# Kernel tuning notes

Measured on AMD Instinct MI355X. Metric: run time of the kernel, lower is better.

The kernel has to match this reference:

```python
import jax, jax.numpy as jnp
import numpy as np

D = 768; H = 12; NL = 8; V = 128
LATENT = 1024; TA = 1000; L = 90; S = 1120; B = 8
PAD_IDX = 0


def sinu_pos(n, dim):
    # ScaledSinusoidalEmbedding basis (scale applied by caller)
    half = dim // 2
    inv_freq = 10000.0 ** (-(jnp.arange(half, dtype=jnp.float32) / half))
    ang = jnp.arange(n, dtype=jnp.float32)[:, None] * inv_freq[None, :]
    return jnp.concatenate([jnp.sin(ang), jnp.cos(ang)], axis=-1)  # [n, dim]


def ln(x, g):
    m = x.mean(-1, keepdims=True)
    v = ((x - m) ** 2).mean(-1, keepdims=True)
    return (x - m) * jax.lax.rsqrt(v + 1e-5) * g


def decoder(x, ln1_g, ln2_g, lnf_g, qkv_w, attn_o_w, fc_w, mlp_o_w):
    Bq, Sq, _ = x.shape
    dh = D // H
    causal = jnp.tril(jnp.ones((Sq, Sq), bool))
    for l in range(NL):
        h = ln(x, ln1_g[l])
        q, k, v = jnp.split(h @ qkv_w[l].T, 3, axis=-1)
        q = q.reshape(Bq, Sq, H, dh).transpose(0, 2, 1, 3)
        k = k.reshape(Bq, Sq, H, dh).transpose(0, 2, 1, 3)
        v = v.reshape(Bq, Sq, H, dh).transpose(0, 2, 1, 3)
        att = jnp.einsum('bhqd,bhkd->bhqk', q, k) / jnp.sqrt(jnp.asarray(dh, x.dtype))
        att = jax.nn.softmax(jnp.where(causal, att, -1e9), axis=-1)
        o = jnp.einsum('bhqk,bhkd->bhqd', att, v).transpose(0, 2, 1, 3).reshape(Bq, Sq, D)
        x = x + o @ attn_o_w[l].T
        h = ln(x, ln2_g[l])
        x = x + jax.nn.gelu(h @ fc_w[l].T, approximate=False) @ mlp_o_w[l].T
    return ln(x, lnf_g)


def setup_inputs() -> dict:
    key = jax.random.key(0)
    ks = iter(jax.random.split(key, 24))
    p = lambda shape: 0.02 * jax.random.normal(next(ks), shape, jnp.float32)
    inp = {}
    inp['audio'] = jax.random.normal(next(ks), (B, TA, LATENT), jnp.float32)
    inp['audio_lengths'] = jax.random.randint(next(ks), (B,), TA // 2, TA + 1)
    ll = jax.random.randint(next(ks), (B,), L // 2, L + 1)
    ll = ll.at[0].set(L)  # labels are padded to max label length in-batch
    inp['label_lengths'] = ll
    lab = jax.random.randint(next(ks), (B, L), 2, V)
    inp['labels'] = jnp.where(jnp.arange(L)[None, :] < ll[:, None], lab, PAD_IDX)
    inp['text_emb_w'] = p((V, D))
    inp['text_head_w'] = p((V, D))
    inp['audio_proj_w'] = p((D, LATENT))
    inp['audio_proj_b'] = jnp.zeros((D,), jnp.float32)
    inp['start_emb'] = p((D,))
    inp['audio_pos_scale'] = jnp.asarray(D ** -0.5, jnp.float32)
    inp['text_pos_scale'] = jnp.asarray(D ** -0.5, jnp.float32)
    inp['ln1_g'] = jnp.ones((NL, D), jnp.float32)
    inp['ln2_g'] = jnp.ones((NL, D), jnp.float32)
    inp['lnf_g'] = jnp.ones((D,), jnp.float32)
    inp['qkv_w'] = p((NL, 3 * D, D))
    inp['attn_o_w'] = p((NL, D, D))
    inp['fc_w'] = p((NL, 4 * D, D))
    inp['mlp_o_w'] = p((NL, D, 4 * D))
    return inp


def reference(audio, labels, audio_lengths, label_lengths, text_emb_w, text_head_w,
              audio_proj_w, audio_proj_b, start_emb, audio_pos_scale, text_pos_scale,
              ln1_g, ln2_g, lnf_g, qkv_w, attn_o_w, fc_w, mlp_o_w):
    # audio projection + scaled sinusoidal positions
    audio_h = audio @ audio_proj_w.T + audio_proj_b                  # [B,TA,D]
    audio_h = audio_h + sinu_pos(TA, D) * audio_pos_scale
    text_h = text_emb_w[labels] + sinu_pos(L, D) * text_pos_scale    # [B,L,D]

    # vectorized ragged packing: [audio[:al] | start_emb | text[:ll-1] | zero-pad] -> [B,S,D]
    pos = jnp.arange(S)[None, :]                                     # [1,S]
    al = audio_lengths[:, None]
    ll = label_lengths[:, None]
    aud = jnp.pad(audio_h, ((0, 0), (0, S - TA), (0, 0)))
    tj = jnp.clip(pos - al - 1, 0, L - 1)                            # text index per slot
    txt = jnp.take_along_axis(text_h, tj[:, :, None], axis=1)
    emb = jnp.where((pos < al)[..., None], aud,
          jnp.where((pos == al)[..., None], start_emb,
          jnp.where((pos < al + ll)[..., None], txt, 0.0)))

    x = decoder(emb, ln1_g, ln2_g, lnf_g, qkv_w, attn_o_w, fc_w, mlp_o_w)

    # gather text latents x[b, al:al+ll] padded to L (== labels.shape[1])
    j = jnp.arange(L)[None, :]
    gi = jnp.clip(al + j, 0, S - 1)
    lat = jnp.take_along_axis(x, gi[:, :, None], axis=1)             # [B,L,D]
    lat = jnp.where((j < ll)[..., None], lat, 0.0)
    logits = lat @ text_head_w.T                                     # [B,L,V]

    # cross entropy, ignore_index = PAD_IDX, mean over non-pad tokens
    logp = jax.nn.log_softmax(logits, axis=-1)
    nll = -jnp.take_along_axis(logp, labels[..., None], axis=-1)[..., 0]
    m = (labels != PAD_IDX).astype(jnp.float32)
    return jnp.sum(nll * m) / jnp.sum(m)
```

## Files before the change

### kernel.cpp

```cpp
#include <hip/hip_runtime.h>

#define D_   768
#define H_   12
#define NL_  8
#define V_   128
#define LAT_ 1024
#define TA_  1000
#define L_   90
#define S_   1120
#define B_   8
#define DH_  64
#define MROWS (B_*S_)

typedef __bf16 bf16x8_t __attribute__((ext_vector_type(8)));
typedef float  f32x4_t  __attribute__((ext_vector_type(4)));

__global__ void sniff_kernel(const void* __restrict__ ones_src,
                             int* __restrict__ flag, float* __restrict__ accum) {
  if (threadIdx.x == 0) {
    unsigned w = *(const unsigned*)ones_src;
    flag[0] = (w == 0x3F803F80u) ? 1 : 0;
    accum[0] = 0.0f;
    accum[1] = 0.0f;
  }
}

__global__ __launch_bounds__(256) void cvt8_kernel(const void* __restrict__ src,
    long off, __bf16* __restrict__ dst, long n8, const int* __restrict__ flag) {
  long i = (long)blockIdx.x * 256 + threadIdx.x;
  const long stride = (long)gridDim.x * 256;
  if (*flag) {
    const bf16x8_t* s = (const bf16x8_t*)((const __bf16*)src + off);
    bf16x8_t* d = (bf16x8_t*)dst;
    for (; i < n8; i += stride) d[i] = s[i];
  } else {
    const float* s = (const float*)src + off;
    for (; i < n8; i += stride) {
      float4 a = *(const float4*)(s + i*8);
      float4 b = *(const float4*)(s + i*8 + 4);
      bf16x8_t v;
      v[0]=(__bf16)a.x; v[1]=(__bf16)a.y; v[2]=(__bf16)a.z; v[3]=(__bf16)a.w;
      v[4]=(__bf16)b.x; v[5]=(__bf16)b.y; v[6]=(__bf16)b.z; v[7]=(__bf16)b.w;
      *(bf16x8_t*)(dst + i*8) = v;
    }
  }
}

__global__ void cvt1_kernel(const void* __restrict__ src, long off,
    __bf16* __restrict__ dst, int n, const int* __restrict__ flag) {
  int i = threadIdx.x;
  if (i < n) {
    if (*flag) dst[i] = ((const __bf16*)src + off)[i];
    else       dst[i] = (__bf16)((const float*)src + off)[i];
  }
}

__device__ __forceinline__ void gload_lds16(const __bf16* g, __bf16* l) {
  __builtin_amdgcn_global_load_lds(
      (const __attribute__((address_space(1))) void*)g,
      (__attribute__((address_space(3))) void*)l, 16, 0, 0);
}

template<int EPI>
__global__ __launch_bounds__(256) void gemm_kernel(
    const __bf16* __restrict__ A, const __bf16* __restrict__ W,
    void* __restrict__ Cout, const __bf16* __restrict__ bias,
    int M, int N, int K)
{
  __shared__ __align__(16) __bf16 As[128*32];
  __shared__ __align__(16) __bf16 Ws[128*32];
  const int tid  = threadIdx.x;
  const int wave = tid >> 6, lane = tid & 63;
  const int wm = wave >> 1, wn = wave & 1;
  const int lrow = lane & 15, lquad = lane >> 4;
  const int bm = blockIdx.y * 128, bn = blockIdx.x * 128;

  const int c0    = wave*2;
  const int srow0 = c0*16 + (lane >> 2);
  const int kc8   = (lane & 3) * 8;
  const int gaA0  = min(bm + srow0,      M-1);
  const int gaA1  = min(bm + srow0 + 16, M-1);
  const size_t a0 = (size_t)gaA0*K + kc8;
  const size_t a1 = (size_t)gaA1*K + kc8;
  const size_t w0 = (size_t)(bn + srow0)*K + kc8;
  const size_t w1 = (size_t)(bn + srow0 + 16)*K + kc8;
  __bf16* ldsA0 = &As[ c0   *512 + lane*8];
  __bf16* ldsA1 = &As[(c0+1)*512 + lane*8];
  __bf16* ldsW0 = &Ws[ c0   *512 + lane*8];
  __bf16* ldsW1 = &Ws[(c0+1)*512 + lane*8];

  f32x4_t acc[4][4] = {};

  for (int kk = 0; kk < K; kk += 32) {
    gload_lds16(&A[a0 + kk], ldsA0);
    gload_lds16(&A[a1 + kk], ldsA1);
    gload_lds16(&W[w0 + kk], ldsW0);
    gload_lds16(&W[w1 + kk], ldsW1);
    __syncthreads();

    bf16x8_t af[4], bfr[4];
    #pragma unroll
    for (int i = 0; i < 4; ++i)
      af[i] = *reinterpret_cast<const bf16x8_t*>(&As[(wm*64 + i*16 + lrow)*32 + lquad*8]);
    #pragma unroll
    for (int j = 0; j < 4; ++j)
      bfr[j] = *reinterpret_cast<const bf16x8_t*>(&Ws[(wn*64 + j*16 + lrow)*32 + lquad*8]);
    #pragma unroll
    for (int i = 0; i < 4; ++i)
      #pragma unroll
      for (int j = 0; j < 4; ++j)
        acc[i][j] = __builtin_amdgcn_mfma_f32_16x16x32_bf16(af[i], bfr[j], acc[i][j], 0, 0, 0);
    __syncthreads();
  }

  const int orow0 = bm + wm*64 + lquad*4;
  const int ocol0 = bn + wn*64 + lrow;
  #pragma unroll
  for (int i = 0; i < 4; ++i) {
    #pragma unroll
    for (int j = 0; j < 4; ++j) {
      #pragma unroll
      for (int r = 0; r < 4; ++r) {
        int row = orow0 + i*16 + r;
        int col = ocol0 + j*16;
        if (row < M) {
          float v = acc[i][j][r];
          if (EPI == 0) {
            ((__bf16*)Cout)[(size_t)row*N + col] = (__bf16)v;
          } else if (EPI == 1) {
            ((float*)Cout)[(size_t)row*N + col] = v + (float)bias[col];
          } else if (EPI == 2) {
            ((float*)Cout)[(size_t)row*N + col] += v;
          } else {
            float gv = 0.5f * v * (1.0f + erff(v * 0.70710678118654752f));
            ((__bf16*)Cout)[(size_t)row*N + col] = (__bf16)gv;
          }
        }
      }
    }
  }
}

template<bool F32OUT>
__global__ __launch_bounds__(256) void ln_kernel(const float* __restrict__ x,
    const __bf16* __restrict__ g, void* __restrict__ outp)
{
  const int row = blockIdx.x;
  const int tid = threadIdx.x;
  const float* xr = x + (size_t)row * D_;
  float v0 = xr[tid], v1 = xr[tid+256], v2 = xr[tid+512];
  float s  = v0+v1+v2;
  float sq = v0*v0 + v1*v1 + v2*v2;
  #pragma unroll
  for (int off = 32; off > 0; off >>= 1) {
    s  += __shfl_down(s,  off);
    sq += __shfl_down(sq, off);
  }
  __shared__ float ps[4], pq[4];
  __shared__ float smean, srstd;
  const int wave = tid >> 6, lane = tid & 63;
  if (lane == 0) { ps[wave] = s; pq[wave] = sq; }
  __syncthreads();
  if (tid == 0) {
    float S4 = ps[0]+ps[1]+ps[2]+ps[3];
    float Q4 = pq[0]+pq[1]+pq[2]+pq[3];
    float mean = S4 * (1.0f/D_);
    float var  = Q4 * (1.0f/D_) - mean*mean;
    smean = mean;
    srstd = rsqrtf(var + 1e-5f);
  }
  __syncthreads();
  const float mean = smean, rstd = srstd;
  if (F32OUT) {
    float* o = (float*)outp + (size_t)row*D_;
    o[tid]     = (v0-mean)*rstd*(float)g[tid];
    o[tid+256] = (v1-mean)*rstd*(float)g[tid+256];
    o[tid+512] = (v2-mean)*rstd*(float)g[tid+512];
  } else {
    __bf16* o = (__bf16*)outp + (size_t)row*D_;
    o[tid]     = (__bf16)((v0-mean)*rstd*(float)g[tid]);
    o[tid+256] = (__bf16)((v1-mean)*rstd*(float)g[tid+256]);
    o[tid+512] = (__bf16)((v2-mean)*rstd*(float)g[tid+512]);
  }
}

__device__ __forceinline__ float sinu_pe(int pindex, int d) {
  int d2 = (d < 384) ? d : d - 384;
  float invf = __expf(-((float)d2 / 384.0f) * 9.210340371976184f);
  float ang  = (float)pindex * invf;
  return (d < 384) ? sinf(ang) : cosf(ang);
}

__global__ __launch_bounds__(256) void embed_kernel(const float* __restrict__ audio_h,
    const int* __restrict__ labels, const int* __restrict__ alen, const int* __restrict__ llen,
    const __bf16* __restrict__ temb, const __bf16* __restrict__ semb,
    const __bf16* __restrict__ aps, const __bf16* __restrict__ tps,
    float* __restrict__ x)
{
  const int bp = blockIdx.x;
  const int b = bp / S_, pos = bp % S_;
  const int a = alen[b], t = llen[b];
  float* xr = x + (size_t)bp * D_;
  if (pos < a) {
    const float apsf = (float)aps[0];
    const float* ar = audio_h + ((size_t)b*TA_ + pos)*D_;
    for (int d = threadIdx.x; d < D_; d += 256)
      xr[d] = ar[d] + sinu_pe(pos, d) * apsf;
  } else if (pos == a) {
    for (int d = threadIdx.x; d < D_; d += 256) xr[d] = (float)semb[d];
  } else if (pos < a + t) {
    const float tpsf = (float)tps[0];
    int tj = pos - a - 1;
    tj = tj < 0 ? 0 : (tj > L_-1 ? L_-1 : tj);
    int tok = labels[b*L_ + tj];
    const __bf16* tr = temb + (size_t)tok * D_;
    for (int d = threadIdx.x; d < D_; d += 256)
      xr[d] = (float)tr[d] + sinu_pe(tj, d) * tpsf;
  } else {
    for (int d = threadIdx.x; d < D_; d += 256) xr[d] = 0.0f;
  }
}

#define KSTR 72
#define VSTR 40
#define PSTR 40

__global__ __launch_bounds__(256) void attn_kernel(const __bf16* __restrict__ qkv,
                                                   __bf16* __restrict__ outp)
{
  __shared__ __align__(16) __bf16 Ks[32*KSTR];
  __shared__ __align__(16) __bf16 Vt[64*VSTR];
  __shared__ __align__(16) __bf16 Ps[4][32*PSTR];
  const int tid  = threadIdx.x;
  const int wave = tid >> 6, lane = tid & 63;
  const int lrow = lane & 15, lquad = lane >> 4;
  const int bh = blockIdx.y;
  const int b = bh / H_, h = bh % H_;
  const int q0 = ((int)gridDim.x - 1 - (int)blockIdx.x) * 128;

  bf16x8_t qf[2][2];
  #pragma unroll
  for (int i = 0; i < 2; ++i) {
    int q = q0 + wave*32 + i*16 + lrow;
    int qc2 = q < S_ ? q : S_-1;
    const __bf16* qp = qkv + ((size_t)(b*S_ + qc2))*(3*D_) + h*DH_;
    #pragma unroll
    for (int kc = 0; kc < 2; ++kc)
      qf[i][kc] = *reinterpret_cast<const bf16x8_t*>(qp + kc*32 + lquad*8);
  }

  f32x4_t o[2][4] = {};
  float m_i[2][4], l_i[2][4];
  #pragma unroll
  for (int i = 0; i < 2; ++i)
    #pragma unroll
    for (int r = 0; r < 4; ++r) { m_i[i][r] = -1e30f; l_i[i][r] = 0.0f; }

  const int kend = min(q0 + 127, S_-1);
  for (int kt = 0; kt <= kend; kt += 32) {
    {
      int j = tid >> 3, d0 = (tid & 7)*8;
      const __bf16* kp = qkv + ((size_t)(b*S_ + kt + j))*(3*D_) + D_ + h*DH_ + d0;
      *reinterpret_cast<bf16x8_t*>(&Ks[j*KSTR + d0]) =
          *reinterpret_cast<const bf16x8_t*>(kp);
      int d = tid & 63, kb = tid >> 6;
      const __bf16* vp = qkv + ((size_t)(b*S_ + kt + kb*8))*(3*D_) + 2*D_ + h*DH_ + d;
      bf16x8_t v8;
      #pragma unroll
      for (int e = 0; e < 8; ++e) v8[e] = vp[(size_t)e*(3*D_)];
      *reinterpret_cast<bf16x8_t*>(&Vt[d*VSTR + kb*8]) = v8;
    }
    __syncthreads();

    bf16x8_t kf[2][2];
    #pragma unroll
    for (int j2 = 0; j2 < 2; ++j2)
      #pragma unroll
      for (int kc = 0; kc < 2; ++kc)
        kf[j2][kc] = *reinterpret_cast<const bf16x8_t*>(
            &Ks[(j2*16 + lrow)*KSTR + kc*32 + lquad*8]);
    f32x4_t s[2][2] = {};
    #pragma unroll
    for (int i = 0; i < 2; ++i)
      #pragma unroll
      for (int j2 = 0; j2 < 2; ++j2) {
        s[i][j2] = __builtin_amdgcn_mfma_f32_16x16x32_bf16(qf[i][0], kf[j2][0], s[i][j2], 0,0,0);
        s[i][j2] = __builtin_amdgcn_mfma_f32_16x16x32_bf16(qf[i][1], kf[j2][1], s[i][j2], 0,0,0);
      }

    #pragma unroll
    for (int i = 0; i < 2; ++i) {
      #pragma unroll
      for (int r = 0; r < 4; ++r) {
        const int qrow = q0 + wave*32 + i*16 + lquad*4 + r;
        float mx = -1e30f;
        #pragma unroll
        for (int j2 = 0; j2 < 2; ++j2) {
          int key = kt + j2*16 + lrow;
          float sv = s[i][j2][r] * 0.125f;
          sv = (key <= qrow) ? sv : -1e30f;
          s[i][j2][r] = sv;
          mx = fmaxf(mx, sv);
        }
        mx = fmaxf(mx, __shfl_xor(mx, 1));
        mx = fmaxf(mx, __shfl_xor(mx, 2));
        mx = fmaxf(mx, __shfl_xor(mx, 4));
        mx = fmaxf(mx, __shfl_xor(mx, 8));
        const float mnew  = fmaxf(m_i[i][r], mx);
        const float alpha = __expf(m_i[i][r] - mnew);
        float psum = 0.0f;
        #pragma unroll
        for (int j2 = 0; j2 < 2; ++j2) {
          float pv = __expf(s[i][j2][r] - mnew);
          s[i][j2][r] = pv;
          psum += pv;
        }
        psum += __shfl_xor(psum, 1);
        psum += __shfl_xor(psum, 2);
        psum += __shfl_xor(psum, 4);
        psum += __shfl_xor(psum, 8);
        l_i[i][r] = l_i[i][r]*alpha + psum;
        m_i[i][r] = mnew;
        #pragma unroll
        for (int n = 0; n < 4; ++n) o[i][n][r] *= alpha;
      }
    }

    __bf16* pw = &Ps[wave][0];
    #pragma unroll
    for (int i = 0; i < 2; ++i)
      #pragma unroll
      for (int j2 = 0; j2 < 2; ++j2)
        #pragma unroll
        for (int r = 0; r < 4; ++r)
          pw[(i*16 + lquad*4 + r)*PSTR + j2*16 + lrow] = (__bf16)s[i][j2][r];
    bf16x8_t pf[2];
    #pragma unroll
    for (int i = 0; i < 2; ++i)
      pf[i] = *reinterpret_cast<const bf16x8_t*>(&pw[(i*16 + lrow)*PSTR + lquad*8]);
    bf16x8_t vf[4];
    #pragma unroll
    for (int n = 0; n < 4; ++n)
      vf[n] = *reinterpret_cast<const bf16x8_t*>(&Vt[(n*16 + lrow)*VSTR + lquad*8]);
    #pragma unroll
    for (int i = 0; i < 2; ++i)
      #pragma unroll
      for (int n = 0; n < 4; ++n)
        o[i][n] = __builtin_amdgcn_mfma_f32_16x16x32_bf16(pf[i], vf[n], o[i][n], 0,0,0);
    __syncthreads();
  }

  #pragma unroll
  for (int i = 0; i < 2; ++i) {
    const int qb = q0 + wave*32 + i*16 + lquad*4;
    #pragma unroll
    for (int r = 0; r < 4; ++r) {
      if (qb + r < S_) {
        float inv = 1.0f / l_i[i][r];
        __bf16* orow = outp + ((size_t)(b*S_ + qb + r))*D_ + h*DH_ + lrow;
        #pragma unroll
        for (int n = 0; n < 4; ++n)
          orow[n*16] = (__bf16)(o[i][n][r] * inv);
      }
    }
  }
}

__global__ __launch_bounds__(128) void head_loss_kernel(const float* __restrict__ xf,
    const int* __restrict__ labels, const int* __restrict__ alen,
    const int* __restrict__ llen, const __bf16* __restrict__ hw,
    float* __restrict__ accum)
{
  const int bj = blockIdx.x;
  const int b = bj / L_, j = bj % L_;
  const int lab = labels[b*L_ + j];
  if (lab == 0) return;
  int gi = alen[b] + j; gi = gi < S_-1 ? gi : S_-1;
  const float* row = xf + ((size_t)(b*S_ + gi))*D_;
  __shared__ float lr[D_];
  for (int d = threadIdx.x; d < D_; d += 128) lr[d] = row[d];
  __syncthreads();
  const int v = threadIdx.x;
  const __bf16* wrow = hw + (size_t)v*D_;
  float dot = 0.0f;
  for (int d = 0; d < D_; d += 8) {
    bf16x8_t w8 = *reinterpret_cast<const bf16x8_t*>(wrow + d);
    #pragma unroll
    for (int e = 0; e < 8; ++e) dot += lr[d+e]*(float)w8[e];
  }
  __shared__ float lg[V_];
  lg[v] = dot;
  __syncthreads();
  if (threadIdx.x == 0) {
    float mx = lg[0];
    for (int i = 1; i < V_; ++i) mx = fmaxf(mx, lg[i]);
    float se = 0.0f;
    for (int i = 0; i < V_; ++i) se += __expf(lg[i]-mx);
    float nll = (mx + logf(se)) - lg[lab];
    atomicAdd(accum, nll);
    atomicAdd(accum+1, 1.0f);
  }
}

__global__ void finalize_kernel(const float* __restrict__ accum,
                                const int* __restrict__ flag, void* __restrict__ out) {
  if (threadIdx.x == 0) {
    float v = accum[0] / accum[1];
    if (*flag) ((__bf16*)out)[0] = (__bf16)v;
    else       ((float*)out)[0]  = v;
  }
}

extern "C" void kernel_launch(void* const* d_in, const int* in_sizes, int n_in,
                              void* d_out, int out_size, void* d_ws, size_t ws_size,
                              hipStream_t stream)
{
  const void* audio        = d_in[0];
  const int*  audio_len    = (const int*)d_in[1];
  const int*  label_len    = (const int*)d_in[2];
  const int*  labels       = (const int*)d_in[3];
  const void* text_emb_w   = d_in[4];
  const void* text_head_w  = d_in[5];
  const void* audio_proj_w = d_in[6];
  const void* audio_proj_b = d_in[7];
  const void* start_emb    = d_in[8];
  const void* aps          = d_in[9];
  const void* tps          = d_in[10];
  const void* ln1_g        = d_in[11];
  const void* ln2_g        = d_in[12];
  const void* lnf_g        = d_in[13];
  const void* qkv_w        = d_in[14];
  const void* attn_o_w     = d_in[15];
  const void* fc_w         = d_in[16];
  const void* mlp_o_w      = d_in[17];

  char* p = (char*)d_ws;
  auto alloc = [&](size_t bytes) {
    char* r = p;
    p += (bytes + 255) & ~(size_t)255;
    return r;
  };
  int*    flag    = (int*)   alloc(64);
  float*  accum   = (float*) alloc(192);
  float*  x       = (float*) alloc((size_t)MROWS*D_*4);
  __bf16* hbuf    = (__bf16*)alloc((size_t)MROWS*D_*2);
  __bf16* qkvbuf  = (__bf16*)alloc((size_t)MROWS*3*D_*2);
  __bf16* attnout = (__bf16*)alloc((size_t)MROWS*D_*2);
  __bf16* ffnbuf  = (__bf16*)alloc((size_t)MROWS*4*D_*2);
  __bf16* wbuf    = (__bf16*)alloc((size_t)4*D_*D_*2);
  __bf16* temb_b  = (__bf16*)alloc((size_t)V_*D_*2);
  __bf16* thead_b = (__bf16*)alloc((size_t)V_*D_*2);
  __bf16* apw_b   = (__bf16*)alloc((size_t)D_*LAT_*2);
  __bf16* apb_b   = (__bf16*)alloc((size_t)D_*2);
  __bf16* semb_b  = (__bf16*)alloc((size_t)D_*2);
  __bf16* aps_b   = (__bf16*)alloc(64);
  __bf16* tps_b   = (__bf16*)alloc(64);
  __bf16* ln1_b   = (__bf16*)alloc((size_t)NL_*D_*2);
  __bf16* ln2_b   = (__bf16*)alloc((size_t)NL_*D_*2);
  __bf16* lnf_b   = (__bf16*)alloc((size_t)D_*2);
  __bf16* audio_bf = qkvbuf;
  float*  audio_h  = (float*)ffnbuf;
  float*  xf       = (float*)ffnbuf;

  auto cvt = [&](const void* src, long off, __bf16* dst, long n) {
    if (n >= 8) {
      long n8 = n >> 3;
      int blocks = (int)((n8 + 255) / 256 < 512 ? (n8 + 255) / 256 : 512);
      cvt8_kernel<<<blocks, 256, 0, stream>>>(src, off, dst, n8, flag);
    } else {
      cvt1_kernel<<<1, 64, 0, stream>>>(src, off, dst, (int)n, flag);
    }
  };

  sniff_kernel<<<1, 64, 0, stream>>>(lnf_g, flag, accum);

  cvt(audio,        0, audio_bf, (long)B_*TA_*LAT_);
  cvt(text_emb_w,   0, temb_b,   (long)V_*D_);
  cvt(text_head_w,  0, thead_b,  (long)V_*D_);
  cvt(audio_proj_w, 0, apw_b,    (long)D_*LAT_);
  cvt(audio_proj_b, 0, apb_b,    D_);
  cvt(start_emb,    0, semb_b,   D_);
  cvt(aps,          0, aps_b,    1);
  cvt(tps,          0, tps_b,    1);
  cvt(ln1_g,        0, ln1_b,    (long)NL_*D_);
  cvt(ln2_g,        0, ln2_b,    (long)NL_*D_);
  cvt(lnf_g,        0, lnf_b,    D_);

  gemm_kernel<1><<<dim3(D_/128, (B_*TA_ + 127)/128), 256, 0, stream>>>(
      audio_bf, apw_b, audio_h, apb_b, B_*TA_, D_, LAT_);
  embed_kernel<<<MROWS, 256, 0, stream>>>(audio_h, labels, audio_len, label_len,
      temb_b, semb_b, aps_b, tps_b, x);

  for (int l = 0; l < NL_; ++l) {
    ln_kernel<false><<<MROWS, 256, 0, stream>>>(x, ln1_b + l*D_, hbuf);
    cvt(qkv_w, (long)l*3*D_*D_, wbuf, (long)3*D_*D_);
    gemm_kernel<0><<<dim3(3*D_/128, MROWS/128), 256, 0, stream>>>(
        hbuf, wbuf, qkvbuf, nullptr, MROWS, 3*D_, D_);
    attn_kernel<<<dim3((S_ + 127)/128, B_*H_), 256, 0, stream>>>(qkvbuf, attnout);
    cvt(attn_o_w, (long)l*D_*D_, wbuf, (long)D_*D_);
    gemm_kernel<2><<<dim3(D_/128, MROWS/128), 256, 0, stream>>>(
        attnout, wbuf, x, nullptr, MROWS, D_, D_);
    ln_kernel<false><<<MROWS, 256, 0, stream>>>(x, ln2_b + l*D_, hbuf);
    cvt(fc_w, (long)l*4*D_*D_, wbuf, (long)4*D_*D_);
    gemm_kernel<3><<<dim3(4*D_/128, MROWS/128), 256, 0, stream>>>(
        hbuf, wbuf, ffnbuf, nullptr, MROWS, 4*D_, D_);
    cvt(mlp_o_w, (long)l*4*D_*D_, wbuf, (long)4*D_*D_);
    gemm_kernel<2><<<dim3(D_/128, MROWS/128), 256, 0, stream>>>(
        ffnbuf, wbuf, x, nullptr, MROWS, D_, 4*D_);
  }

  ln_kernel<true><<<MROWS, 256, 0, stream>>>(x, lnf_b, xf);
  head_loss_kernel<<<B_*L_, 128, 0, stream>>>(xf, labels, audio_len, label_len,
                                              thead_b, accum);
  finalize_kernel<<<1, 64, 0, stream>>>(accum, flag, d_out);
}
```

Measured before the change: 3.704 ms.

## Fuse fp32-to-bf16 conversion into GEMM loads and vectorize V transpose

The separate conversion kernels for the audio input and every layer's weights are removed. The GEMM now reads fp32 directly and packs it to bf16 on the way into LDS, chosen at runtime by a dtype flag, which avoids an extra read/write pass and a launch per weight matrix. The attention kernel now loads V with one vector load per thread and scatters it transposed into LDS with a narrower stride, replacing eight strided scalar global loads. In exchange, the fp32 path loses the async global-to-LDS load and rereads the fp32 weights in every row tile, doubling operand bytes. The narrower stride may also cause LDS bank conflicts.

```diff
diff --git a/kernel.cpp b/kernel.cpp
--- a/kernel.cpp
+++ b/kernel.cpp
@@ -61,11 +61,19 @@
       (__attribute__((address_space(3))) void*)l, 16, 0, 0);
 }
 
-template<int EPI>
+__device__ __forceinline__ bf16x8_t pack8(const float* s) {
+  float4 a = *(const float4*)s, b = *(const float4*)(s + 4);
+  bf16x8_t v;
+  v[0]=(__bf16)a.x; v[1]=(__bf16)a.y; v[2]=(__bf16)a.z; v[3]=(__bf16)a.w;
+  v[4]=(__bf16)b.x; v[5]=(__bf16)b.y; v[6]=(__bf16)b.z; v[7]=(__bf16)b.w;
+  return v;
+}
+
+template<int EPI, bool AEXT, bool WEXT>
 __global__ __launch_bounds__(256) void gemm_kernel(
-    const __bf16* __restrict__ A, const __bf16* __restrict__ W,
+    const void* __restrict__ A, const void* __restrict__ W, long woff,
     void* __restrict__ Cout, const __bf16* __restrict__ bias,
-    int M, int N, int K)
+    const int* __restrict__ flag, int M, int N, int K)
 {
   __shared__ __align__(16) __bf16 As[128*32];
   __shared__ __align__(16) __bf16 Ws[128*32];
@@ -74,6 +82,14 @@
   const int wm = wave >> 1, wn = wave & 1;
   const int lrow = lane & 15, lquad = lane >> 4;
   const int bm = blockIdx.y * 128, bn = blockIdx.x * 128;
+
+  const int fl = *flag;
+  const bool af32 = AEXT && (fl == 0);
+  const bool wf32 = WEXT && (fl == 0);
+  const __bf16* Ab = (const __bf16*)A;
+  const float*  Af = (const float*)A;
+  const __bf16* Wb = (const __bf16*)W + woff;
+  const float*  Wf = (const float*)W + woff;
 
   const int c0    = wave*2;
   const int srow0 = c0*16 + (lane >> 2);
@@ -92,10 +108,20 @@
   f32x4_t acc[4][4] = {};
 
   for (int kk = 0; kk < K; kk += 32) {
-    gload_lds16(&A[a0 + kk], ldsA0);
-    gload_lds16(&A[a1 + kk], ldsA1);
-    gload_lds16(&W[w0 + kk], ldsW0);
-    gload_lds16(&W[w1 + kk], ldsW1);
+    if (!af32) {
+      gload_lds16(&Ab[a0 + kk], ldsA0);
+      gload_lds16(&Ab[a1 + kk], ldsA1);
+    } else {
+      *(bf16x8_t*)ldsA0 = pack8(&Af[a0 + kk]);
+      *(bf16x8_t*)ldsA1 = pack8(&Af[a1 + kk]);
+    }
+    if (!wf32) {
+      gload_lds16(&Wb[w0 + kk], ldsW0);
+      gload_lds16(&Wb[w1 + kk], ldsW1);
+    } else {
+      *(bf16x8_t*)ldsW0 = pack8(&Wf[w0 + kk]);
+      *(bf16x8_t*)ldsW1 = pack8(&Wf[w1 + kk]);
+    }
     __syncthreads();
 
     bf16x8_t af[4], bfr[4];
@@ -222,7 +248,7 @@
 }
 
 #define KSTR 72
-#define VSTR 40
+#define VSTR 34
 #define PSTR 40
 
 __global__ __launch_bounds__(256) void attn_kernel(const __bf16* __restrict__ qkv,
@@ -263,12 +289,10 @@
       const __bf16* kp = qkv + ((size_t)(b*S_ + kt + j))*(3*D_) + D_ + h*DH_ + d0;
       *reinterpret_cast<bf16x8_t*>(&Ks[j*KSTR + d0]) =
           *reinterpret_cast<const bf16x8_t*>(kp);
-      int d = tid & 63, kb = tid >> 6;
-      const __bf16* vp = qkv + ((size_t)(b*S_ + kt + kb*8))*(3*D_) + 2*D_ + h*DH_ + d;
-      bf16x8_t v8;
-      #pragma unroll
-      for (int e = 0; e < 8; ++e) v8[e] = vp[(size_t)e*(3*D_)];
-      *reinterpret_cast<bf16x8_t*>(&Vt[d*VSTR + kb*8]) = v8;
+      bf16x8_t v8 = *reinterpret_cast<const bf16x8_t*>(kp + D_);
+      #pragma unroll
+      for (int e = 0; e < 8; ++e)
+        Vt[(d0+e)*VSTR + j] = v8[e];
     }
     __syncthreads();
 
@@ -447,10 +471,8 @@
   __bf16* qkvbuf  = (__bf16*)alloc((size_t)MROWS*3*D_*2);
   __bf16* attnout = (__bf16*)alloc((size_t)MROWS*D_*2);
   __bf16* ffnbuf  = (__bf16*)alloc((size_t)MROWS*4*D_*2);
-  __bf16* wbuf    = (__bf16*)alloc((size_t)4*D_*D_*2);
   __bf16* temb_b  = (__bf16*)alloc((size_t)V_*D_*2);
   __bf16* thead_b = (__bf16*)alloc((size_t)V_*D_*2);
-  __bf16* apw_b   = (__bf16*)alloc((size_t)D_*LAT_*2);
   __bf16* apb_b   = (__bf16*)alloc((size_t)D_*2);
   __bf16* semb_b  = (__bf16*)alloc((size_t)D_*2);
   __bf16* aps_b   = (__bf16*)alloc(64);
@@ -458,7 +480,6 @@
   __bf16* ln1_b   = (__bf16*)alloc((size_t)NL_*D_*2);
   __bf16* ln2_b   = (__bf16*)alloc((size_t)NL_*D_*2);
   __bf16* lnf_b   = (__bf16*)alloc((size_t)D_*2);
-  __bf16* audio_bf = qkvbuf;
   float*  audio_h  = (float*)ffnbuf;
   float*  xf       = (float*)ffnbuf;
 
@@ -474,10 +495,8 @@
 
   sniff_kernel<<<1, 64, 0, stream>>>(lnf_g, flag, accum);
 
-  cvt(audio,        0, audio_bf, (long)B_*TA_*LAT_);
   cvt(text_emb_w,   0, temb_b,   (long)V_*D_);
   cvt(text_head_w,  0, thead_b,  (long)V_*D_);
-  cvt(audio_proj_w, 0, apw_b,    (long)D_*LAT_);
   cvt(audio_proj_b, 0, apb_b,    D_);
   cvt(start_emb,    0, semb_b,   D_);
   cvt(aps,          0, aps_b,    1);
@@ -486,27 +505,23 @@
   cvt(ln2_g,        0, ln2_b,    (long)NL_*D_);
   cvt(lnf_g,        0, lnf_b,    D_);
 
-  gemm_kernel<1><<<dim3(D_/128, (B_*TA_ + 127)/128), 256, 0, stream>>>(
-      audio_bf, apw_b, audio_h, apb_b, B_*TA_, D_, LAT_);
+  gemm_kernel<1, true, true><<<dim3(D_/128, (B_*TA_ + 127)/128), 256, 0, stream>>>(
+      audio, audio_proj_w, 0, audio_h, apb_b, flag, B_*TA_, D_, LAT_);
   embed_kernel<<<MROWS, 256, 0, stream>>>(audio_h, labels, audio_len, label_len,
       temb_b, semb_b, aps_b, tps_b, x);
 
   for (int l = 0; l < NL_; ++l) {
     ln_kernel<false><<<MROWS, 256, 0, stream>>>(x, ln1_b + l*D_, hbuf);
-    cvt(qkv_w, (long)l*3*D_*D_, wbuf, (long)3*D_*D_);
-    gemm_kernel<0><<<dim3(3*D_/128, MROWS/128), 256, 0, stream>>>(
-        hbuf, wbuf, qkvbuf, nullptr, MROWS, 3*D_, D_);
+    gemm_kernel<0, false, true><<<dim3(3*D_/128, MROWS/128), 256, 0, stream>>>(
+        hbuf, qkv_w, (long)l*3*D_*D_, qkvbuf, nullptr, flag, MROWS, 3*D_, D_);
     attn_kernel<<<dim3((S_ + 127)/128, B_*H_), 256, 0, stream>>>(qkvbuf, attnout);
-    cvt(attn_o_w, (long)l*D_*D_, wbuf, (long)D_*D_);
-    gemm_kernel<2><<<dim3(D_/128, MROWS/128), 256, 0, stream>>>(
-        attnout, wbuf, x, nullptr, MROWS, D_, D_);
+    gemm_kernel<2, false, true><<<dim3(D_/128, MROWS/128), 256, 0, stream>>>(
+        attnout, attn_o_w, (long)l*D_*D_, x, nullptr, flag, MROWS, D_, D_);
     ln_kernel<false><<<MROWS, 256, 0, stream>>>(x, ln2_b + l*D_, hbuf);
-    cvt(fc_w, (long)l*4*D_*D_, wbuf, (long)4*D_*D_);
-    gemm_kernel<3><<<dim3(4*D_/128, MROWS/128), 256, 0, stream>>>(
-        hbuf, wbuf, ffnbuf, nullptr, MROWS, 4*D_, D_);
-    cvt(mlp_o_w, (long)l*4*D_*D_, wbuf, (long)4*D_*D_);
-    gemm_kernel<2><<<dim3(D_/128, MROWS/128), 256, 0, stream>>>(
-        ffnbuf, wbuf, x, nullptr, MROWS, D_, 4*D_);
+    gemm_kernel<3, false, true><<<dim3(4*D_/128, MROWS/128), 256, 0, stream>>>(
+        hbuf, fc_w, (long)l*4*D_*D_, ffnbuf, nullptr, flag, MROWS, 4*D_, D_);
+    gemm_kernel<2, false, true><<<dim3(D_/128, MROWS/128), 256, 0, stream>>>(
+        ffnbuf, mlp_o_w, (long)l*4*D_*D_, x, nullptr, flag, MROWS, D_, 4*D_);
   }
 
   ln_kernel<true><<<MROWS, 256, 0, stream>>>(x, lnf_b, xf);
```

After: 4.295 ms. 16.0% more time.
